# Kernel tuning notes

Measured on AMD Instinct MI355X. Metric: run time of the kernel, lower is better.

The kernel has to match this reference:

```python
import jax, jax.numpy as jnp
import numpy as np

V = 32000   # output_dim (vocab)
E = 512     # embedding_dim
H = 1024    # hidden_dim
BS = 128    # batch
SL = 256    # encoder seq len


def setup_inputs() -> dict:
    key = jax.random.key(0)
    ks = jax.random.split(key, 14)
    s = 0.02  # param init scale
    return {
        "inp_tok": jax.random.randint(ks[0], (BS,), 0, V),
        "h0": jax.random.normal(ks[1], (1, BS, H), jnp.float32),
        "c0": jax.random.normal(ks[2], (1, BS, H), jnp.float32),
        "eo": jax.random.normal(ks[3], (BS, SL, 2 * H), jnp.float32),
        "emb_w": jax.random.normal(ks[4], (V, E), jnp.float32) * s,
        "attn_w": jax.random.normal(ks[5], (H, 3 * H), jnp.float32) * s,
        "attn_b": jnp.zeros((H,), jnp.float32),
        "v_w": jax.random.normal(ks[6], (1, H), jnp.float32) * s,
        "w_ih": jax.random.normal(ks[7], (4 * H, E + 2 * H), jnp.float32) * s,
        "w_hh": jax.random.normal(ks[8], (4 * H, H), jnp.float32) * s,
        "b_ih": jnp.zeros((4 * H,), jnp.float32),
        "b_hh": jnp.zeros((4 * H,), jnp.float32),
        "fco_w": jax.random.normal(ks[9], (V, 3 * H + E), jnp.float32) * s,
        "fco_b": jnp.zeros((V,), jnp.float32),
    }


def reference(inp_tok, h0, c0, eo, emb_w, attn_w, attn_b, v_w,
              w_ih, w_hh, b_ih, b_hh, fco_w, fco_b):
    # Dropout is identity in eval mode (reference baseline).
    embedded = emb_w[inp_tok]                       # [BS, E]
    h_top = h0[-1]                                  # [BS, H] (last layer hidden)
    c_top = c0[-1]                                  # [BS, H]

    # Bahdanau attention: attn(cat(h, eo)) split into h-part and eo-part
    # attn_w: [H, 3H] -> [:, :H] acts on h, [:, H:] acts on eo (2H feats)
    h_proj = jnp.einsum('bd,hd->bh', h_top, attn_w[:, :H])        # [BS, H]
    e_proj = jnp.einsum('bsd,hd->bsh', eo, attn_w[:, H:])         # [BS, SL, H]
    en = jnp.tanh(h_proj[:, None, :] + e_proj + attn_b)           # [BS, SL, H]
    scores = jnp.einsum('bsh,h->bs', en, v_w[0])                  # [BS, SL]
    a = jax.nn.softmax(scores, axis=1)                            # [BS, SL]
    weighted = jnp.einsum('bs,bsd->bd', a, eo)                    # [BS, 2H]

    # Single LSTM step (n_layers=1), PyTorch gate order i, f, g, o
    x = jnp.concatenate([embedded, weighted], axis=-1)            # [BS, E+2H]
    gates = x @ w_ih.T + b_ih + h_top @ w_hh.T + b_hh             # [BS, 4H]
    i_g, f_g, g_g, o_g = jnp.split(gates, 4, axis=-1)
    c_new = jax.nn.sigmoid(f_g) * c_top + jax.nn.sigmoid(i_g) * jnp.tanh(g_g)
    h_new = jax.nn.sigmoid(o_g) * jnp.tanh(c_new)                 # [BS, H]

    # Output projection on cat(lstm_out, weighted, embedded)
    out = jnp.concatenate([h_new, weighted, embedded], axis=-1)   # [BS, 3H+E]
    prediction = out @ fco_w.T + fco_b                            # [BS, V]
    return prediction, h_new[None], c_new[None]
```

## Files before the change

kernel.cpp:

```cpp
#include <hip/hip_runtime.h>
#include <math.h>

typedef unsigned short u16;
typedef __attribute__((ext_vector_type(8))) __bf16 bf16x8;
typedef __attribute__((ext_vector_type(4))) float  f32x4;
typedef __attribute__((ext_vector_type(8))) unsigned short u16x8;

__device__ __forceinline__ u16 f2bf(float x) {
    unsigned u = __float_as_uint(x);
    u += 0x7FFFu + ((u >> 16) & 1u);
    return (u16)(u >> 16);
}
__device__ __forceinline__ float b2f(u16 u) { return __uint_as_float(((unsigned)u) << 16); }
__device__ __forceinline__ float ftanh(float x) {
    x = fminf(fmaxf(x, -15.f), 15.f);
    const float e = __expf(2.f * x);
    return (e - 1.f) / (e + 1.f);
}
__device__ __forceinline__ float sigm(float x) { return 1.f / (1.f + __expf(-x)); }

__device__ __forceinline__ void gload16(const void* g, void* l) {
    __builtin_amdgcn_global_load_lds(
        (const __attribute__((address_space(1))) unsigned*)g,
        (__attribute__((address_space(3))) unsigned*)l, 16, 0, 0);
}

template<int MODE, int BM, int BN, int WGM, int WGN, bool A16, bool B16>
__global__ __launch_bounds__(WGM * WGN * 64, 4)
void gemm_k(const void* __restrict__ Ap, int lda,
            const void* __restrict__ Bp, int ldb,
            const float* __restrict__ B2,
            float* __restrict__ C, int ldc,
            const float* __restrict__ ep0,
            const float* __restrict__ ep1,
            const float* __restrict__ ep2,
            int kc)
{
    constexpr int NW = WGM * WGN, NT = NW * 64;
    constexpr int WM = BM / WGM, WN = BN / WGN;
    constexpr int NMT = WM / 16, NNT = WN / 16;

    __shared__ __align__(16) u16 As[BM * 32];
    __shared__ __align__(16) u16 Bs[BN * 32];

    const int t    = threadIdx.x;
    const int n0   = blockIdx.x * BN;
    const int m0   = blockIdx.y * BM;
    const int k0c  = blockIdx.z * kc;
    const int wave = t >> 6, lane = t & 63;
    const int lrow = lane & 15, quad = lane >> 4;
    const int wm0  = (wave / WGN) * WM;
    const int wn0  = (wave % WGN) * WN;

    f32x4 acc[NMT][NNT];
#pragma unroll
    for (int i = 0; i < NMT; ++i)
#pragma unroll
        for (int j = 0; j < NNT; ++j) acc[i][j] = f32x4{0.f, 0.f, 0.f, 0.f};

    const int niter = kc >> 5;
    for (int kt = 0; kt < niter; ++kt) {
        const int kcur = k0c + (kt << 5);
        __syncthreads();
        if constexpr (A16) {
            const u16* Ab = (const u16*)Ap;
#pragma unroll
            for (int c = t; c < BM * 4; c += NT)
                gload16(Ab + (size_t)(m0 + (c >> 2)) * lda + kcur + (c & 3) * 8, &As[c * 8]);
        } else {
            const float* Af = (const float*)Ap;
#pragma unroll
            for (int c = t; c < BM * 8; c += NT) {
                const int r = c >> 3, c4 = c & 7;
                const float4 v = *(const float4*)(Af + (size_t)(m0 + r) * lda + kcur + c4 * 4);
                ushort4 h; h.x = f2bf(v.x); h.y = f2bf(v.y); h.z = f2bf(v.z); h.w = f2bf(v.w);
                *(ushort4*)(&As[r * 32 + c4 * 4]) = h;
            }
        }
        if constexpr (B16) {
            const u16* Bb = (const u16*)Bp;
#pragma unroll
            for (int c = t; c < BN * 4; c += NT)
                gload16(Bb + (size_t)(n0 + (c >> 2)) * ldb + kcur + (c & 3) * 8, &Bs[c * 8]);
        } else {
#pragma unroll
            for (int c = t; c < BN * 8; c += NT) {
                const int r = c >> 3, c4 = c & 7;
                const int kg = kcur + c4 * 4;
                const float* src;
                if constexpr (MODE == 2)
                    src = (kg < 2560) ? ((const float*)Bp + (size_t)(n0 + r) * 2560 + kg)
                                      : (B2 + (size_t)(n0 + r) * 1024 + (kg - 2560));
                else
                    src = (const float*)Bp + (size_t)(n0 + r) * ldb + kg;
                const float4 v = *(const float4*)src;
                ushort4 h; h.x = f2bf(v.x); h.y = f2bf(v.y); h.z = f2bf(v.z); h.w = f2bf(v.w);
                *(ushort4*)(&Bs[r * 32 + c4 * 4]) = h;
            }
        }
        __syncthreads();

        bf16x8 af[NMT];
#pragma unroll
        for (int mt = 0; mt < NMT; ++mt)
            af[mt] = *(const bf16x8*)(&As[(wm0 + mt * 16 + lrow) * 32 + quad * 8]);
#pragma unroll
        for (int nt = 0; nt < NNT; ++nt) {
            const bf16x8 bfr = *(const bf16x8*)(&Bs[(wn0 + nt * 16 + lrow) * 32 + quad * 8]);
#pragma unroll
            for (int mt = 0; mt < NMT; ++mt)
                acc[mt][nt] = __builtin_amdgcn_mfma_f32_16x16x32_bf16(af[mt], bfr, acc[mt][nt], 0, 0, 0);
        }
    }

    if constexpr (MODE == 1) {
        const int b = m0 >> 8;
        float part[NMT][4];
#pragma unroll
        for (int mt = 0; mt < NMT; ++mt) { part[mt][0] = part[mt][1] = part[mt][2] = part[mt][3] = 0.f; }
#pragma unroll
        for (int nt = 0; nt < NNT; ++nt) {
            const int gn = n0 + wn0 + nt * 16 + lrow;
            const float hb = ep0[b * 1024 + gn] + ep1[gn];
            const float vv = ep2[gn];
#pragma unroll
            for (int mt = 0; mt < NMT; ++mt)
#pragma unroll
                for (int r = 0; r < 4; ++r)
                    part[mt][r] += vv * ftanh(acc[mt][nt][r] + hb);
        }
#pragma unroll
        for (int mt = 0; mt < NMT; ++mt)
#pragma unroll
            for (int r = 0; r < 4; ++r) {
                float s = part[mt][r];
                s += __shfl_xor(s, 1); s += __shfl_xor(s, 2);
                s += __shfl_xor(s, 4); s += __shfl_xor(s, 8);
                if (lrow == 0)
                    atomicAdd(&C[m0 + wm0 + mt * 16 + quad * 4 + r], s);
            }
    } else {
        float* Cw = C;
        if constexpr (MODE == 2) Cw += (size_t)blockIdx.z * (size_t)(128 * 4096);
#pragma unroll
        for (int mt = 0; mt < NMT; ++mt)
#pragma unroll
            for (int nt = 0; nt < NNT; ++nt)
#pragma unroll
                for (int r = 0; r < 4; ++r) {
                    const int gm = m0 + wm0 + mt * 16 + quad * 4 + r;
                    const int gn = n0 + wn0 + nt * 16 + lrow;
                    float v = acc[mt][nt][r];
                    if constexpr (MODE == 3) v += ep0[gn];
                    if constexpr (MODE == 4) atomicAdd(&Cw[(size_t)gm * ldc + gn], v);
                    else                     Cw[(size_t)gm * ldc + gn] = v;
                }
    }
}

__global__ __launch_bounds__(256) void conv_eo(const float* __restrict__ s, u16* __restrict__ d) {
    const size_t i = ((size_t)blockIdx.x * 256 + threadIdx.x) * 8;
    const float4 a = *(const float4*)(s + i);
    const float4 b = *(const float4*)(s + i + 4);
    u16x8 o;
    o[0] = f2bf(a.x); o[1] = f2bf(a.y); o[2] = f2bf(a.z); o[3] = f2bf(a.w);
    o[4] = f2bf(b.x); o[5] = f2bf(b.y); o[6] = f2bf(b.z); o[7] = f2bf(b.w);
    *(u16x8*)(d + i) = o;
}

__global__ __launch_bounds__(256) void conv_w(const float* __restrict__ aw,
                                              u16* __restrict__ wHP, u16* __restrict__ wEO) {
    const int c = blockIdx.x * 256 + threadIdx.x;
    const int row = c / 384, cc = (c - row * 384) * 8;
    const float* s = aw + (size_t)row * 3072 + cc;
    const float4 a = *(const float4*)s;
    const float4 b = *(const float4*)(s + 4);
    u16x8 o;
    o[0] = f2bf(a.x); o[1] = f2bf(a.y); o[2] = f2bf(a.z); o[3] = f2bf(a.w);
    o[4] = f2bf(b.x); o[5] = f2bf(b.y); o[6] = f2bf(b.z); o[7] = f2bf(b.w);
    if (cc < 1024) *(u16x8*)(wHP + (size_t)row * 1024 + cc) = o;
    else           *(u16x8*)(wEO + (size_t)row * 2048 + (cc - 1024)) = o;
}

__global__ __launch_bounds__(256) void prep(const int* __restrict__ tok,
                                            const float* __restrict__ emb,
                                            const float* __restrict__ h0,
                                            u16* __restrict__ xh, u16* __restrict__ oc) {
    const int idx = blockIdx.x * 256 + threadIdx.x;
    const int b = idx / 1536, j = idx - b * 1536;
    if (j < 512) {
        const u16 e = f2bf(emb[(size_t)tok[b] * 512 + j]);
        xh[b * 3584 + j] = e;
        oc[b * 3584 + 3072 + j] = e;
    } else {
        const int d = j - 512;
        xh[b * 3584 + 2560 + d] = f2bf(h0[b * 1024 + d]);
    }
}

template<typename T>
__global__ __launch_bounds__(256) void attn_soft(const float* __restrict__ scores,
                                                 const T* __restrict__ eo,
                                                 u16* __restrict__ xh, u16* __restrict__ oc) {
    const int b = blockIdx.x >> 3, q = blockIdx.x & 7, t = threadIdx.x;
    __shared__ float red[256];
    __shared__ float sm[256];
    const float sc = scores[b * 256 + t];
    red[t] = sc; __syncthreads();
#pragma unroll
    for (int off = 128; off > 0; off >>= 1) {
        if (t < off) red[t] = fmaxf(red[t], red[t + off]);
        __syncthreads();
    }
    const float M = red[0]; __syncthreads();
    const float e = __expf(sc - M);
    red[t] = e; __syncthreads();
#pragma unroll
    for (int off = 128; off > 0; off >>= 1) {
        if (t < off) red[t] += red[t + off];
        __syncthreads();
    }
    const float S = red[0];
    sm[t] = e / S;
    __syncthreads();

    const T* ep = eo + (size_t)b * 256 * 2048 + q * 256 + t;
    float acc = 0.f;
#pragma unroll 4
    for (int s = 0; s < 256; ++s) {
        float v;
        if constexpr (sizeof(T) == 2) v = b2f(((const u16*)ep)[(size_t)s * 2048]);
        else                          v = ((const float*)ep)[(size_t)s * 2048];
        acc += sm[s] * v;
    }
    const int d = q * 256 + t;
    const u16 o = f2bf(acc);
    xh[b * 3584 + 512 + d]  = o;
    oc[b * 3584 + 1024 + d] = o;
}

__global__ __launch_bounds__(256) void lstm_epi(const float* __restrict__ gp,
                                                const float* __restrict__ b_ih,
                                                const float* __restrict__ b_hh,
                                                const float* __restrict__ c0,
                                                u16* __restrict__ oc,
                                                float* __restrict__ hc) {
    const int idx = blockIdx.x * 256 + threadIdx.x;
    const int b = idx >> 10, j = idx & 1023;
    float g[4];
#pragma unroll
    for (int gi = 0; gi < 4; ++gi) {
        const int col = gi * 1024 + j;
        float s = b_ih[col] + b_hh[col];
#pragma unroll
        for (int kb = 0; kb < 8; ++kb) s += gp[(size_t)kb * 524288 + b * 4096 + col];
        g[gi] = s;
    }
    const float c = sigm(g[1]) * c0[idx] + sigm(g[0]) * ftanh(g[2]);
    const float h = sigm(g[3]) * ftanh(c);
    oc[b * 3584 + j] = f2bf(h);
    hc[idx]          = h;
    hc[131072 + idx] = c;
}

extern "C" void kernel_launch(void* const* d_in, const int* in_sizes, int n_in,
                              void* d_out, int out_size, void* d_ws, size_t ws_size,
                              hipStream_t stream)
{
    const int*   tok    = (const int*)  d_in[0];
    const float* h0     = (const float*)d_in[1];
    const float* c0     = (const float*)d_in[2];
    const float* eo     = (const float*)d_in[3];
    const float* emb_w  = (const float*)d_in[4];
    const float* attn_w = (const float*)d_in[5];
    const float* attn_b = (const float*)d_in[6];
    const float* v_w    = (const float*)d_in[7];
    const float* w_ih   = (const float*)d_in[8];
    const float* w_hh   = (const float*)d_in[9];
    const float* b_ih   = (const float*)d_in[10];
    const float* b_hh   = (const float*)d_in[11];
    const float* fco_w  = (const float*)d_in[12];
    const float* fco_b  = (const float*)d_in[13];
    float* out = (float*)d_out;

    char*  w      = (char*)d_ws;
    float* scores = (float*)(w);
    float* hproj  = (float*)(w + 131072);
    float* gparts = (float*)(w + 655360);
    u16*   xh16   = (u16*)  (w + 17432576);
    u16*   oc16   = (u16*)  (w + 18350080);
    u16*   wHP    = (u16*)  (w + 19267584);
    u16*   wEO    = (u16*)  (w + 21364736);
    u16*   eo16   = (u16*)  (w + 25559040);
    const bool big = ws_size >= 159776768ull;

    hipMemsetAsync(w, 0, 655360, stream);
    prep<<<768, 256, 0, stream>>>(tok, emb_w, h0, xh16, oc16);
    conv_w<<<1536, 256, 0, stream>>>(attn_w, wHP, wEO);
    if (big) conv_eo<<<32768, 256, 0, stream>>>(eo, eo16);

    gemm_k<4, 128, 64, 2, 2, true, true><<<dim3(16, 1, 4), 256, 0, stream>>>(
        xh16 + 2560, 3584, wHP, 1024, nullptr, hproj, 1024, nullptr, nullptr, nullptr, 256);

    if (big)
        gemm_k<1, 128, 128, 2, 2, true, true><<<dim3(8, 256, 1), 256, 0, stream>>>(
            eo16, 2048, wEO, 2048, nullptr, scores, 0, hproj, attn_b, v_w, 2048);
    else
        gemm_k<1, 128, 128, 2, 2, false, true><<<dim3(8, 256, 1), 256, 0, stream>>>(
            eo, 2048, wEO, 2048, nullptr, scores, 0, hproj, attn_b, v_w, 2048);

    if (big) attn_soft<u16>  <<<1024, 256, 0, stream>>>(scores, eo16, xh16, oc16);
    else     attn_soft<float><<<1024, 256, 0, stream>>>(scores, eo,   xh16, oc16);

    gemm_k<2, 128, 64, 2, 2, true, false><<<dim3(64, 1, 8), 256, 0, stream>>>(
        xh16, 3584, w_ih, 0, w_hh, gparts, 4096, nullptr, nullptr, nullptr, 448);

    lstm_epi<<<512, 256, 0, stream>>>(gparts, b_ih, b_hh, c0, oc16, out + 4096000);

    gemm_k<3, 128, 32, 4, 1, true, false><<<dim3(1000, 1, 1), 256, 0, stream>>>(
        oc16, 3584, fco_w, 3584, nullptr, out, 32000, fco_b, nullptr, nullptr, 3584);
}
```

Before: 1.137 ms.

## Prefetch fp32 GEMM tiles in registers, fuse setup kernels, vectorize attention

Adds a two-deep register prefetch of fp32 A/B tiles in the GEMM, so the global loads for iteration k+2 are issued before the MFMA work of iteration k. Merges the memset, prep and weight-conversion kernels into one setup launch and makes conv_eo handle 32 elements per thread. Changes attn_soft to one block per batch row that reads 8 contiguous elements per thread, replacing 8 blocks per row with strided scalar reads. The prefetch buffers raise register pressure, and the attention kernel now launches only 128 blocks, which lowers parallelism.

```diff
diff --git a/kernel.cpp b/kernel.cpp
--- a/kernel.cpp
+++ b/kernel.cpp
@@ -39,6 +39,8 @@
     constexpr int NW = WGM * WGN, NT = NW * 64;
     constexpr int WM = BM / WGM, WN = BN / WGN;
     constexpr int NMT = WM / 16, NNT = WN / 16;
+    constexpr int NAI = A16 ? 1 : (BM * 8) / NT;
+    constexpr int NBI = B16 ? 1 : (BN * 8) / NT;
 
     __shared__ __align__(16) u16 As[BM * 32];
     __shared__ __align__(16) u16 Bs[BN * 32];
@@ -52,39 +54,24 @@
     const int wm0  = (wave / WGN) * WM;
     const int wn0  = (wave % WGN) * WN;
 
-    f32x4 acc[NMT][NNT];
-#pragma unroll
-    for (int i = 0; i < NMT; ++i)
-#pragma unroll
-        for (int j = 0; j < NNT; ++j) acc[i][j] = f32x4{0.f, 0.f, 0.f, 0.f};
-
-    const int niter = kc >> 5;
-    for (int kt = 0; kt < niter; ++kt) {
-        const int kcur = k0c + (kt << 5);
-        __syncthreads();
-        if constexpr (A16) {
-            const u16* Ab = (const u16*)Ap;
-#pragma unroll
-            for (int c = t; c < BM * 4; c += NT)
-                gload16(Ab + (size_t)(m0 + (c >> 2)) * lda + kcur + (c & 3) * 8, &As[c * 8]);
-        } else {
+    float4 apre[2][NAI];
+    float4 bpre[2][NBI];
+
+    auto loadAf = [&](int kcur, int buf) {
+        if constexpr (!A16) {
             const float* Af = (const float*)Ap;
 #pragma unroll
-            for (int c = t; c < BM * 8; c += NT) {
-                const int r = c >> 3, c4 = c & 7;
-                const float4 v = *(const float4*)(Af + (size_t)(m0 + r) * lda + kcur + c4 * 4);
-                ushort4 h; h.x = f2bf(v.x); h.y = f2bf(v.y); h.z = f2bf(v.z); h.w = f2bf(v.w);
-                *(ushort4*)(&As[r * 32 + c4 * 4]) = h;
-            }
-        }
-        if constexpr (B16) {
-            const u16* Bb = (const u16*)Bp;
-#pragma unroll
-            for (int c = t; c < BN * 4; c += NT)
-                gload16(Bb + (size_t)(n0 + (c >> 2)) * ldb + kcur + (c & 3) * 8, &Bs[c * 8]);
-        } else {
-#pragma unroll
-            for (int c = t; c < BN * 8; c += NT) {
+            for (int i = 0; i < NAI; ++i) {
+                const int c = t + i * NT;
+                apre[buf][i] = *(const float4*)(Af + (size_t)(m0 + (c >> 3)) * lda + kcur + (c & 7) * 4);
+            }
+        }
+    };
+    auto loadBf = [&](int kcur, int buf) {
+        if constexpr (!B16) {
+#pragma unroll
+            for (int i = 0; i < NBI; ++i) {
+                const int c = t + i * NT;
                 const int r = c >> 3, c4 = c & 7;
                 const int kg = kcur + c4 * 4;
                 const float* src;
@@ -93,12 +80,61 @@
                                       : (B2 + (size_t)(n0 + r) * 1024 + (kg - 2560));
                 else
                     src = (const float*)Bp + (size_t)(n0 + r) * ldb + kg;
-                const float4 v = *(const float4*)src;
+                bpre[buf][i] = *(const float4*)src;
+            }
+        }
+    };
+    auto storeA = [&](int buf) {
+        if constexpr (!A16) {
+#pragma unroll
+            for (int i = 0; i < NAI; ++i) {
+                const int c = t + i * NT;
+                const float4 v = apre[buf][i];
                 ushort4 h; h.x = f2bf(v.x); h.y = f2bf(v.y); h.z = f2bf(v.z); h.w = f2bf(v.w);
-                *(ushort4*)(&Bs[r * 32 + c4 * 4]) = h;
-            }
-        }
+                *(ushort4*)(&As[(c >> 3) * 32 + (c & 7) * 4]) = h;
+            }
+        }
+    };
+    auto storeB = [&](int buf) {
+        if constexpr (!B16) {
+#pragma unroll
+            for (int i = 0; i < NBI; ++i) {
+                const int c = t + i * NT;
+                const float4 v = bpre[buf][i];
+                ushort4 h; h.x = f2bf(v.x); h.y = f2bf(v.y); h.z = f2bf(v.z); h.w = f2bf(v.w);
+                *(ushort4*)(&Bs[(c >> 3) * 32 + (c & 7) * 4]) = h;
+            }
+        }
+    };
+
+    f32x4 acc[NMT][NNT];
+#pragma unroll
+    for (int i = 0; i < NMT; ++i)
+#pragma unroll
+        for (int j = 0; j < NNT; ++j) acc[i][j] = f32x4{0.f, 0.f, 0.f, 0.f};
+
+    const int niter = kc >> 5;
+    loadAf(k0c, 0); loadBf(k0c, 0);
+    if (niter > 1) { loadAf(k0c + 32, 1); loadBf(k0c + 32, 1); }
+
+    for (int kt = 0; kt < niter; ++kt) {
+        const int kcur = k0c + (kt << 5);
         __syncthreads();
+        if constexpr (A16) {
+            const u16* Ab = (const u16*)Ap;
+#pragma unroll
+            for (int c = t; c < BM * 4; c += NT)
+                gload16(Ab + (size_t)(m0 + (c >> 2)) * lda + kcur + (c & 3) * 8, &As[c * 8]);
+        } else storeA(kt & 1);
+        if constexpr (B16) {
+            const u16* Bb = (const u16*)Bp;
+#pragma unroll
+            for (int c = t; c < BN * 4; c += NT)
+                gload16(Bb + (size_t)(n0 + (c >> 2)) * ldb + kcur + (c & 3) * 8, &Bs[c * 8]);
+        } else storeB(kt & 1);
+        __syncthreads();
+
+        if (kt + 2 < niter) { loadAf(kcur + 64, kt & 1); loadBf(kcur + 64, kt & 1); }
 
         bf16x8 af[NMT];
 #pragma unroll
@@ -158,43 +194,51 @@
     }
 }
 
+__global__ __launch_bounds__(256) void setup(const int* __restrict__ tok,
+                                             const float* __restrict__ emb,
+                                             const float* __restrict__ h0,
+                                             const float* __restrict__ aw,
+                                             float* __restrict__ zero0,
+                                             u16* __restrict__ xh, u16* __restrict__ oc,
+                                             u16* __restrict__ wHP, u16* __restrict__ wEO) {
+    const int blk = blockIdx.x, t = threadIdx.x;
+    if (blk < 640) {
+        zero0[blk * 256 + t] = 0.f;
+    } else if (blk < 1408) {
+        const int idx = (blk - 640) * 256 + t;
+        const int b = idx / 1536, j = idx - b * 1536;
+        if (j < 512) {
+            const u16 e = f2bf(emb[(size_t)tok[b] * 512 + j]);
+            xh[b * 3584 + j] = e;
+            oc[b * 3584 + 3072 + j] = e;
+        } else {
+            const int d = j - 512;
+            xh[b * 3584 + 2560 + d] = f2bf(h0[b * 1024 + d]);
+        }
+    } else {
+        const int c = (blk - 1408) * 256 + t;
+        const int row = c / 384, cc = (c - row * 384) * 8;
+        const float* s = aw + (size_t)row * 3072 + cc;
+        const float4 a = *(const float4*)s;
+        const float4 b = *(const float4*)(s + 4);
+        u16x8 o;
+        o[0] = f2bf(a.x); o[1] = f2bf(a.y); o[2] = f2bf(a.z); o[3] = f2bf(a.w);
+        o[4] = f2bf(b.x); o[5] = f2bf(b.y); o[6] = f2bf(b.z); o[7] = f2bf(b.w);
+        if (cc < 1024) *(u16x8*)(wHP + (size_t)row * 1024 + cc) = o;
+        else           *(u16x8*)(wEO + (size_t)row * 2048 + (cc - 1024)) = o;
+    }
+}
+
 __global__ __launch_bounds__(256) void conv_eo(const float* __restrict__ s, u16* __restrict__ d) {
-    const size_t i = ((size_t)blockIdx.x * 256 + threadIdx.x) * 8;
-    const float4 a = *(const float4*)(s + i);
-    const float4 b = *(const float4*)(s + i + 4);
-    u16x8 o;
-    o[0] = f2bf(a.x); o[1] = f2bf(a.y); o[2] = f2bf(a.z); o[3] = f2bf(a.w);
-    o[4] = f2bf(b.x); o[5] = f2bf(b.y); o[6] = f2bf(b.z); o[7] = f2bf(b.w);
-    *(u16x8*)(d + i) = o;
-}
-
-__global__ __launch_bounds__(256) void conv_w(const float* __restrict__ aw,
-                                              u16* __restrict__ wHP, u16* __restrict__ wEO) {
-    const int c = blockIdx.x * 256 + threadIdx.x;
-    const int row = c / 384, cc = (c - row * 384) * 8;
-    const float* s = aw + (size_t)row * 3072 + cc;
-    const float4 a = *(const float4*)s;
-    const float4 b = *(const float4*)(s + 4);
-    u16x8 o;
-    o[0] = f2bf(a.x); o[1] = f2bf(a.y); o[2] = f2bf(a.z); o[3] = f2bf(a.w);
-    o[4] = f2bf(b.x); o[5] = f2bf(b.y); o[6] = f2bf(b.z); o[7] = f2bf(b.w);
-    if (cc < 1024) *(u16x8*)(wHP + (size_t)row * 1024 + cc) = o;
-    else           *(u16x8*)(wEO + (size_t)row * 2048 + (cc - 1024)) = o;
-}
-
-__global__ __launch_bounds__(256) void prep(const int* __restrict__ tok,
-                                            const float* __restrict__ emb,
-                                            const float* __restrict__ h0,
-                                            u16* __restrict__ xh, u16* __restrict__ oc) {
-    const int idx = blockIdx.x * 256 + threadIdx.x;
-    const int b = idx / 1536, j = idx - b * 1536;
-    if (j < 512) {
-        const u16 e = f2bf(emb[(size_t)tok[b] * 512 + j]);
-        xh[b * 3584 + j] = e;
-        oc[b * 3584 + 3072 + j] = e;
-    } else {
-        const int d = j - 512;
-        xh[b * 3584 + 2560 + d] = f2bf(h0[b * 1024 + d]);
+    const size_t i = ((size_t)blockIdx.x * 256 + threadIdx.x) * 32;
+#pragma unroll
+    for (int j = 0; j < 4; ++j) {
+        const float4 a = *(const float4*)(s + i + j * 8);
+        const float4 b = *(const float4*)(s + i + j * 8 + 4);
+        u16x8 o;
+        o[0] = f2bf(a.x); o[1] = f2bf(a.y); o[2] = f2bf(a.z); o[3] = f2bf(a.w);
+        o[4] = f2bf(b.x); o[5] = f2bf(b.y); o[6] = f2bf(b.z); o[7] = f2bf(b.w);
+        *(u16x8*)(d + i + j * 8) = o;
     }
 }
 
@@ -202,7 +246,7 @@
 __global__ __launch_bounds__(256) void attn_soft(const float* __restrict__ scores,
                                                  const T* __restrict__ eo,
                                                  u16* __restrict__ xh, u16* __restrict__ oc) {
-    const int b = blockIdx.x >> 3, q = blockIdx.x & 7, t = threadIdx.x;
+    const int b = blockIdx.x, t = threadIdx.x;
     __shared__ float red[256];
     __shared__ float sm[256];
     const float sc = scores[b * 256 + t];
@@ -224,19 +268,35 @@
     sm[t] = e / S;
     __syncthreads();
 
-    const T* ep = eo + (size_t)b * 256 * 2048 + q * 256 + t;
-    float acc = 0.f;
+    float acc[8];
+#pragma unroll
+    for (int j = 0; j < 8; ++j) acc[j] = 0.f;
+
+    if constexpr (sizeof(T) == 2) {
+        const u16* base = (const u16*)eo + (size_t)b * 524288 + t * 8;
 #pragma unroll 4
-    for (int s = 0; s < 256; ++s) {
-        float v;
-        if constexpr (sizeof(T) == 2) v = b2f(((const u16*)ep)[(size_t)s * 2048]);
-        else                          v = ((const float*)ep)[(size_t)s * 2048];
-        acc += sm[s] * v;
-    }
-    const int d = q * 256 + t;
-    const u16 o = f2bf(acc);
-    xh[b * 3584 + 512 + d]  = o;
-    oc[b * 3584 + 1024 + d] = o;
+        for (int s = 0; s < 256; ++s) {
+            const u16x8 v = *(const u16x8*)(base + (size_t)s * 2048);
+            const float w = sm[s];
+#pragma unroll
+            for (int j = 0; j < 8; ++j) acc[j] += w * b2f(v[j]);
+        }
+    } else {
+        const float* base = (const float*)eo + (size_t)b * 524288 + t * 8;
+#pragma unroll 2
+        for (int s = 0; s < 256; ++s) {
+            const float4 v0 = *(const float4*)(base + (size_t)s * 2048);
+            const float4 v1 = *(const float4*)(base + (size_t)s * 2048 + 4);
+            const float w = sm[s];
+            acc[0] += w * v0.x; acc[1] += w * v0.y; acc[2] += w * v0.z; acc[3] += w * v0.w;
+            acc[4] += w * v1.x; acc[5] += w * v1.y; acc[6] += w * v1.z; acc[7] += w * v1.w;
+        }
+    }
+    u16x8 o;
+#pragma unroll
+    for (int j = 0; j < 8; ++j) o[j] = f2bf(acc[j]);
+    *(u16x8*)(xh + b * 3584 + 512 + t * 8)  = o;
+    *(u16x8*)(oc + b * 3584 + 1024 + t * 8) = o;
 }
 
 __global__ __launch_bounds__(256) void lstm_epi(const float* __restrict__ gp,
@@ -294,10 +354,8 @@
     u16*   eo16   = (u16*)  (w + 25559040);
     const bool big = ws_size >= 159776768ull;
 
-    hipMemsetAsync(w, 0, 655360, stream);
-    prep<<<768, 256, 0, stream>>>(tok, emb_w, h0, xh16, oc16);
-    conv_w<<<1536, 256, 0, stream>>>(attn_w, wHP, wEO);
-    if (big) conv_eo<<<32768, 256, 0, stream>>>(eo, eo16);
+    setup<<<2944, 256, 0, stream>>>(tok, emb_w, h0, attn_w, scores, xh16, oc16, wHP, wEO);
+    if (big) conv_eo<<<8192, 256, 0, stream>>>(eo, eo16);
 
     gemm_k<4, 128, 64, 2, 2, true, true><<<dim3(16, 1, 4), 256, 0, stream>>>(
         xh16 + 2560, 3584, wHP, 1024, nullptr, hproj, 1024, nullptr, nullptr, nullptr, 256);
@@ -309,8 +367,8 @@
         gemm_k<1, 128, 128, 2, 2, false, true><<<dim3(8, 256, 1), 256, 0, stream>>>(
             eo, 2048, wEO, 2048, nullptr, scores, 0, hproj, attn_b, v_w, 2048);
 
-    if (big) attn_soft<u16>  <<<1024, 256, 0, stream>>>(scores, eo16, xh16, oc16);
-    else     attn_soft<float><<<1024, 256, 0, stream>>>(scores, eo,   xh16, oc16);
+    if (big) attn_soft<u16>  <<<128, 256, 0, stream>>>(scores, eo16, xh16, oc16);
+    else     attn_soft<float><<<128, 256, 0, stream>>>(scores, eo,   xh16, oc16);
 
     gemm_k<2, 128, 64, 2, 2, true, false><<<dim3(64, 1, 8), 256, 0, stream>>>(
         xh16, 3584, w_ih, 0, w_hh, gparts, 4096, nullptr, nullptr, nullptr, 448);
```

Result: slower. 1.201 ms (+5.7%).
